# Kernel tuning notes

Measured on AMD Instinct MI355X. Metric: run time of the kernel, lower is better.

The kernel has to match this reference:

```python
import jax, jax.numpy as jnp
import numpy as np
import math

HIDDEN = 128
NUM_HEADS = 8
HEAD_DIM = HIDDEN // NUM_HEADS
B, L = 2, 512


def setup_inputs() -> dict:
    key = jax.random.key(0)
    ks = jax.random.split(key, 14)
    s = 1.0 / math.sqrt(HIDDEN)
    return {
        "x": jax.random.normal(ks[0], (B, L, HIDDEN), jnp.float32),
        "time_k": jax.random.normal(ks[1], (B, L, L, HIDDEN), jnp.float32) * 0.1,
        "time_v": jax.random.normal(ks[2], (B, L, L, HIDDEN), jnp.float32) * 0.1,
        "abs_pos_k": jax.random.normal(ks[3], (B, L, HIDDEN), jnp.float32),
        "abs_pos_v": jax.random.normal(ks[4], (B, L, HIDDEN), jnp.float32),
        "attn_mask": jax.random.normal(ks[5], (B, 1, L, L), jnp.float32),
        "Wq": jax.random.normal(ks[6], (HIDDEN, HIDDEN), jnp.float32) * s,
        "bq": jnp.zeros((HIDDEN,), jnp.float32),
        "Wk": jax.random.normal(ks[7], (HIDDEN, HIDDEN), jnp.float32) * s,
        "bk": jnp.zeros((HIDDEN,), jnp.float32),
        "Wv": jax.random.normal(ks[8], (HIDDEN, HIDDEN), jnp.float32) * s,
        "bv": jnp.zeros((HIDDEN,), jnp.float32),
        "Wo": jax.random.normal(ks[9], (HIDDEN, HIDDEN), jnp.float32) * s,
        "bo": jnp.zeros((HIDDEN,), jnp.float32),
    }


def _split_heads(t):  # [B,L,H] -> [B,nh,L,hd]
    b, l, _ = t.shape
    return t.reshape(b, l, NUM_HEADS, HEAD_DIM).transpose(0, 2, 1, 3)


def reference(x, time_k, time_v, abs_pos_k, abs_pos_v, attn_mask,
              Wq, bq, Wk, bk, Wv, bv, Wo, bo):
    b, l, h = x.shape
    q = _split_heads(x @ Wq + bq)
    k = _split_heads(x @ Wk + bk)
    v = _split_heads(x @ Wv + bv)
    abs_k = _split_heads(abs_pos_k)
    abs_v = _split_heads(abs_pos_v)
    # time biases: [B,L,L,H] -> [B,nh,Lq,Lk,hd]
    tk = time_k.reshape(b, l, l, NUM_HEADS, HEAD_DIM).transpose(0, 3, 1, 2, 4)
    tv = time_v.reshape(b, l, l, NUM_HEADS, HEAD_DIM).transpose(0, 3, 1, 2, 4)
    scores = (
        jnp.einsum("bhqd,bhkd->bhqk", q, k)
        + jnp.einsum("bhqd,bhkd->bhqk", q, abs_k)
        + jnp.einsum("bhqd,bhqkd->bhqk", q, tk)
    ) / math.sqrt(HEAD_DIM)
    scores = scores + attn_mask
    probs = jax.nn.softmax(scores, axis=-1)  # dropout_prob=0 -> identity
    ctx = (
        jnp.einsum("bhqk,bhkd->bhqd", probs, v)
        + jnp.einsum("bhqk,bhkd->bhqd", probs, abs_v)
        + jnp.einsum("bhqk,bhqkd->bhqd", probs, tv)
    )
    ctx = ctx.transpose(0, 2, 1, 3).reshape(b, l, h)
    return ctx @ Wo + bo
```

## Files before the change

kernel.cpp:

```cpp
#include <hip/hip_runtime.h>

#define BB 2
#define LL 512
#define HH 128
#define NH 8
#define SP_STRIDE 9

typedef float f32x4 __attribute__((ext_vector_type(4)));

__global__ __launch_bounds__(128) void qkv_proj_kernel(
    const float* __restrict__ x,
    const float* __restrict__ abs_pos_k,
    const float* __restrict__ abs_pos_v,
    const float* __restrict__ Wq, const float* __restrict__ bq,
    const float* __restrict__ Wk, const float* __restrict__ bk,
    const float* __restrict__ Wv, const float* __restrict__ bv,
    float* __restrict__ q, float* __restrict__ kp, float* __restrict__ vp)
{
    const int r0 = blockIdx.x * 4;
    const int c = threadIdx.x;
    __shared__ float xs[4][HH];
    #pragma unroll
    for (int r = 0; r < 4; ++r) xs[r][c] = x[(r0 + r) * HH + c];
    __syncthreads();
    float aq[4], ak[4], av[4];
    #pragma unroll
    for (int r = 0; r < 4; ++r) { aq[r] = bq[c]; ak[r] = bk[c]; av[r] = bv[c]; }
    #pragma unroll 4
    for (int i = 0; i < HH; ++i) {
        const float wq = Wq[i * HH + c];
        const float wk = Wk[i * HH + c];
        const float wv = Wv[i * HH + c];
        #pragma unroll
        for (int r = 0; r < 4; ++r) {
            const float xv = xs[r][i];
            aq[r] = fmaf(xv, wq, aq[r]);
            ak[r] = fmaf(xv, wk, ak[r]);
            av[r] = fmaf(xv, wv, av[r]);
        }
    }
    #pragma unroll
    for (int r = 0; r < 4; ++r) {
        const int idx = (r0 + r) * HH + c;
        q[idx]  = aq[r];
        kp[idx] = ak[r] + abs_pos_k[idx];
        vp[idx] = av[r] + abs_pos_v[idx];
    }
}

__global__ __launch_bounds__(256) void attn_fused_kernel(
    const float* __restrict__ q,
    const float* __restrict__ kp,
    const float* __restrict__ vp,
    const float* __restrict__ time_k,
    const float* __restrict__ time_v,
    const float* __restrict__ mask,
    const float* __restrict__ Wo,
    const float* __restrict__ bo,
    float* __restrict__ out)
{
    const int blk = blockIdx.x;
    const int b   = blk >> 9;
    const int qi  = blk & (LL - 1);
    const int t   = threadIdx.x;
    const int c4  = t & 31;
    const int kis = t >> 5;
    const int h   = c4 >> 2;

    __shared__ float s_p[LL * SP_STRIDE];
    __shared__ float s_q[HH];
    __shared__ float s_red[8][HH];
    __shared__ float s_ctx[HH];
    __shared__ float s_inv[NH];

    if (t < HH) s_q[t] = q[(b * LL + qi) * HH + t];
    __syncthreads();

    const float4 q4 = ((const float4*)s_q)[c4];
    const f32x4* __restrict__ tk4 = (const f32x4*)(time_k + (size_t)(b * LL + qi) * (size_t)(LL * HH));
    const float4* __restrict__ kq4 = (const float4*)(kp + (size_t)b * (size_t)(LL * HH));
    const float*  __restrict__ mrow = mask + (size_t)(b * LL + qi) * LL;

    #pragma unroll 8
    for (int kb = 0; kb < LL / 8; ++kb) {
        const int ki = kb * 8 + kis;
        const f32x4  a  = __builtin_nontemporal_load(tk4 + ki * 32 + c4);
        const float4 bk = kq4[ki * 32 + c4];
        float part = q4.x * (a.x + bk.x) + q4.y * (a.y + bk.y)
                   + q4.z * (a.z + bk.z) + q4.w * (a.w + bk.w);
        part += __shfl_xor(part, 1);
        part += __shfl_xor(part, 2);
        if ((c4 & 3) == 0)
            s_p[ki * SP_STRIDE + h] = part;
    }
    __syncthreads();

    {
        const int hh  = t >> 5;
        const int l32 = t & 31;
        float v[LL / 32];
        float m = -1e30f;
        #pragma unroll
        for (int j = 0; j < LL / 32; ++j) {
            const int ki = l32 + j * 32;
            v[j] = s_p[ki * SP_STRIDE + hh] * 0.25f + mrow[ki];
            m = fmaxf(m, v[j]);
        }
        #pragma unroll
        for (int off = 16; off; off >>= 1) m = fmaxf(m, __shfl_xor(m, off));
        float sum = 0.f;
        #pragma unroll
        for (int j = 0; j < LL / 32; ++j) {
            const float e = __expf(v[j] - m);
            s_p[(l32 + j * 32) * SP_STRIDE + hh] = e;
            sum += e;
        }
        #pragma unroll
        for (int off = 16; off; off >>= 1) sum += __shfl_xor(sum, off);
        if (l32 == 0) s_inv[hh] = 1.0f / sum;
    }
    __syncthreads();

    const f32x4* __restrict__ tv4 = (const f32x4*)(time_v + (size_t)(b * LL + qi) * (size_t)(LL * HH));
    const float4* __restrict__ vq4 = (const float4*)(vp + (size_t)b * (size_t)(LL * HH));
    float4 acc = make_float4(0.f, 0.f, 0.f, 0.f);
    #pragma unroll 8
    for (int kb = 0; kb < LL / 8; ++kb) {
        const int ki = kb * 8 + kis;
        const float p = s_p[ki * SP_STRIDE + h];
        const f32x4  a  = __builtin_nontemporal_load(tv4 + ki * 32 + c4);
        const float4 bv = vq4[ki * 32 + c4];
        acc.x = fmaf(p, a.x + bv.x, acc.x);
        acc.y = fmaf(p, a.y + bv.y, acc.y);
        acc.z = fmaf(p, a.z + bv.z, acc.z);
        acc.w = fmaf(p, a.w + bv.w, acc.w);
    }
    const float inv = s_inv[h];
    ((float4*)s_red)[kis * 32 + c4] = make_float4(acc.x * inv, acc.y * inv, acc.z * inv, acc.w * inv);
    __syncthreads();

    if (t < HH) {
        float cv = 0.f;
        #pragma unroll
        for (int r = 0; r < 8; ++r) cv += s_red[r][t];
        s_ctx[t] = cv;
    }
    __syncthreads();

    {
        const int to   = t & (HH - 1);
        const int half = t >> 7;
        float o = half ? 0.f : bo[to];
        const int i0 = half * (HH / 2);
        #pragma unroll 4
        for (int i = i0; i < i0 + HH / 2; ++i)
            o = fmaf(s_ctx[i], Wo[i * HH + to], o);
        __syncthreads();
        s_red[half][to] = o;
    }
    __syncthreads();
    if (t < HH)
        out[(b * LL + qi) * HH + t] = s_red[0][t] + s_red[1][t];
}

extern "C" void kernel_launch(void* const* d_in, const int* in_sizes, int n_in,
                              void* d_out, int out_size, void* d_ws, size_t ws_size,
                              hipStream_t stream) {
    const float* x         = (const float*)d_in[0];
    const float* time_k    = (const float*)d_in[1];
    const float* time_v    = (const float*)d_in[2];
    const float* abs_pos_k = (const float*)d_in[3];
    const float* abs_pos_v = (const float*)d_in[4];
    const float* attn_mask = (const float*)d_in[5];
    const float* Wq = (const float*)d_in[6];
    const float* bq = (const float*)d_in[7];
    const float* Wk = (const float*)d_in[8];
    const float* bk = (const float*)d_in[9];
    const float* Wv = (const float*)d_in[10];
    const float* bv = (const float*)d_in[11];
    const float* Wo = (const float*)d_in[12];
    const float* bo = (const float*)d_in[13];
    float* out = (float*)d_out;

    float* q  = (float*)d_ws;
    float* kp = q  + BB * LL * HH;
    float* vp = kp + BB * LL * HH;

    qkv_proj_kernel<<<BB * LL / 4, 128, 0, stream>>>(
        x, abs_pos_k, abs_pos_v, Wq, bq, Wk, bk, Wv, bv, q, kp, vp);

    attn_fused_kernel<<<BB * LL, 256, 0, stream>>>(
        q, kp, vp, time_k, time_v, attn_mask, Wo, bo, out);
}
```

Before: 531.5 us.

## Split fused attention into score, context and output-projection kernels across key halves

Breaks the fused per-query kernel into three kernels. The score and context kernels each split the key dimension into two halves, which doubles the block count, and the raw scores and partial contexts are staged through workspace memory. The aim is more parallelism and memory-level concurrency when streaming the large time_k/time_v tensors. In exchange it adds two kernel launches and global round trips for the scores (8 MB) and partial contexts, and the softmax is recomputed in both halves. The fused kernel is kept as a fallback when the workspace is too small.

```diff
diff --git a/kernel.cpp b/kernel.cpp
--- a/kernel.cpp
+++ b/kernel.cpp
@@ -46,6 +46,176 @@
         kp[idx] = ak[r] + abs_pos_k[idx];
         vp[idx] = av[r] + abs_pos_v[idx];
     }
+}
+
+__global__ __launch_bounds__(256) void score_kernel(
+    const float* __restrict__ q,
+    const float* __restrict__ kp,
+    const float* __restrict__ time_k,
+    float* __restrict__ scores)
+{
+    const int half = blockIdx.x & 1;
+    const int row  = blockIdx.x >> 1;
+    const int b    = row >> 9;
+    const int t    = threadIdx.x;
+    const int c4   = t & 31;
+    const int kis  = t >> 5;
+    const int h    = c4 >> 2;
+
+    __shared__ float s_q[HH];
+    __shared__ float s_p[(LL / 2) * SP_STRIDE];
+
+    if (t < HH) s_q[t] = q[row * HH + t];
+    __syncthreads();
+
+    const float4 q4 = ((const float4*)s_q)[c4];
+    const f32x4*  __restrict__ tk4 = (const f32x4*)(time_k
+        + (size_t)row * (size_t)(LL * HH) + (size_t)half * (LL / 2) * HH);
+    const float4* __restrict__ kq4 = (const float4*)(kp
+        + (size_t)b * (size_t)(LL * HH) + (size_t)half * (LL / 2) * HH);
+
+    #pragma unroll 8
+    for (int kb = 0; kb < LL / 2 / 8; ++kb) {
+        const int ki = kb * 8 + kis;
+        const f32x4  a  = __builtin_nontemporal_load(tk4 + ki * 32 + c4);
+        const float4 bk = kq4[ki * 32 + c4];
+        float part = q4.x * (a.x + bk.x) + q4.y * (a.y + bk.y)
+                   + q4.z * (a.z + bk.z) + q4.w * (a.w + bk.w);
+        part += __shfl_xor(part, 1);
+        part += __shfl_xor(part, 2);
+        if ((c4 & 3) == 0)
+            s_p[ki * SP_STRIDE + h] = part;
+    }
+    __syncthreads();
+
+    float buf[8];
+    #pragma unroll
+    for (int j = 0; j < 8; ++j) {
+        const int idx = t * 8 + j;
+        buf[j] = s_p[(idx >> 3) * SP_STRIDE + (idx & 7)];
+    }
+    float4* dst = (float4*)(scores + (size_t)row * (LL * NH) + half * (LL / 2) * NH + t * 8);
+    dst[0] = make_float4(buf[0], buf[1], buf[2], buf[3]);
+    dst[1] = make_float4(buf[4], buf[5], buf[6], buf[7]);
+}
+
+__global__ __launch_bounds__(256) void ctx_kernel(
+    const float* __restrict__ scores,
+    const float* __restrict__ vp,
+    const float* __restrict__ time_v,
+    const float* __restrict__ mask,
+    float* __restrict__ pctx)
+{
+    const int half = blockIdx.x & 1;
+    const int row  = blockIdx.x >> 1;
+    const int b    = row >> 9;
+    const int t    = threadIdx.x;
+    const int c4   = t & 31;
+    const int kis  = t >> 5;
+    const int h    = c4 >> 2;
+
+    __shared__ float s_p[LL * SP_STRIDE];
+    __shared__ float s_red[8][HH];
+    __shared__ float s_inv[NH];
+
+    {
+        const float4* src = (const float4*)(scores + (size_t)row * (LL * NH));
+        #pragma unroll
+        for (int j = 0; j < 4; ++j) {
+            const float4 v4 = src[t * 4 + j];
+            const int idx = t * 16 + j * 4;
+            s_p[((idx + 0) >> 3) * SP_STRIDE + ((idx + 0) & 7)] = v4.x;
+            s_p[((idx + 1) >> 3) * SP_STRIDE + ((idx + 1) & 7)] = v4.y;
+            s_p[((idx + 2) >> 3) * SP_STRIDE + ((idx + 2) & 7)] = v4.z;
+            s_p[((idx + 3) >> 3) * SP_STRIDE + ((idx + 3) & 7)] = v4.w;
+        }
+    }
+    __syncthreads();
+
+    {
+        const float* __restrict__ mrow = mask + (size_t)row * LL;
+        const int hh  = t >> 5;
+        const int l32 = t & 31;
+        float v[LL / 32];
+        float m = -1e30f;
+        #pragma unroll
+        for (int j = 0; j < LL / 32; ++j) {
+            const int ki = l32 + j * 32;
+            v[j] = s_p[ki * SP_STRIDE + hh] * 0.25f + mrow[ki];
+            m = fmaxf(m, v[j]);
+        }
+        #pragma unroll
+        for (int off = 16; off; off >>= 1) m = fmaxf(m, __shfl_xor(m, off));
+        float sum = 0.f;
+        #pragma unroll
+        for (int j = 0; j < LL / 32; ++j) {
+            const float e = __expf(v[j] - m);
+            s_p[(l32 + j * 32) * SP_STRIDE + hh] = e;
+            sum += e;
+        }
+        #pragma unroll
+        for (int off = 16; off; off >>= 1) sum += __shfl_xor(sum, off);
+        if (l32 == 0) s_inv[hh] = 1.0f / sum;
+    }
+    __syncthreads();
+
+    const f32x4*  __restrict__ tv4 = (const f32x4*)(time_v
+        + (size_t)row * (size_t)(LL * HH) + (size_t)half * (LL / 2) * HH);
+    const float4* __restrict__ vq4 = (const float4*)(vp
+        + (size_t)b * (size_t)(LL * HH) + (size_t)half * (LL / 2) * HH);
+    float4 acc = make_float4(0.f, 0.f, 0.f, 0.f);
+    #pragma unroll 8
+    for (int kb = 0; kb < LL / 2 / 8; ++kb) {
+        const int ki = kb * 8 + kis;
+        const float p = s_p[(half * (LL / 2) + ki) * SP_STRIDE + h];
+        const f32x4  a  = __builtin_nontemporal_load(tv4 + ki * 32 + c4);
+        const float4 bv = vq4[ki * 32 + c4];
+        acc.x = fmaf(p, a.x + bv.x, acc.x);
+        acc.y = fmaf(p, a.y + bv.y, acc.y);
+        acc.z = fmaf(p, a.z + bv.z, acc.z);
+        acc.w = fmaf(p, a.w + bv.w, acc.w);
+    }
+    const float inv = s_inv[h];
+    ((float4*)s_red)[kis * 32 + c4] = make_float4(acc.x * inv, acc.y * inv, acc.z * inv, acc.w * inv);
+    __syncthreads();
+
+    if (t < HH) {
+        float cv = 0.f;
+        #pragma unroll
+        for (int r = 0; r < 8; ++r) cv += s_red[r][t];
+        pctx[(size_t)half * (BB * LL * HH) + (size_t)row * HH + t] = cv;
+    }
+}
+
+__global__ __launch_bounds__(256) void out_proj_kernel(
+    const float* __restrict__ pctx,
+    const float* __restrict__ Wo,
+    const float* __restrict__ bo,
+    float* __restrict__ out)
+{
+    const int row = blockIdx.x;
+    const int t   = threadIdx.x;
+    __shared__ float s_ctx[HH];
+    __shared__ float s_red[2][HH];
+
+    if (t < HH)
+        s_ctx[t] = pctx[(size_t)row * HH + t]
+                 + pctx[(size_t)(BB * LL * HH) + (size_t)row * HH + t];
+    __syncthreads();
+
+    {
+        const int to   = t & (HH - 1);
+        const int half = t >> 7;
+        float o = half ? 0.f : bo[to];
+        const int i0 = half * (HH / 2);
+        #pragma unroll 4
+        for (int i = i0; i < i0 + HH / 2; ++i)
+            o = fmaf(s_ctx[i], Wo[i * HH + to], o);
+        s_red[half][to] = o;
+    }
+    __syncthreads();
+    if (t < HH)
+        out[(size_t)row * HH + t] = s_red[0][t] + s_red[1][t];
 }
 
 __global__ __launch_bounds__(256) void attn_fused_kernel(
@@ -189,6 +359,17 @@
     qkv_proj_kernel<<<BB * LL / 4, 128, 0, stream>>>(
         x, abs_pos_k, abs_pos_v, Wq, bq, Wk, bk, Wv, bv, q, kp, vp);
 
-    attn_fused_kernel<<<BB * LL, 256, 0, stream>>>(
-        q, kp, vp, time_k, time_v, attn_mask, Wo, bo, out);
-}
+    const size_t need = (size_t)(3 * BB * LL * HH
+                               + (size_t)BB * LL * LL * NH
+                               + 2 * BB * LL * HH) * 4;
+    if (ws_size >= need) {
+        float* scores = vp + BB * LL * HH;
+        float* pctx   = scores + (size_t)BB * LL * LL * NH;
+        score_kernel<<<BB * LL * 2, 256, 0, stream>>>(q, kp, time_k, scores);
+        ctx_kernel<<<BB * LL * 2, 256, 0, stream>>>(scores, vp, time_v, attn_mask, pctx);
+        out_proj_kernel<<<BB * LL, 256, 0, stream>>>(pctx, Wo, bo, out);
+    } else {
+        attn_fused_kernel<<<BB * LL, 256, 0, stream>>>(
+            q, kp, vp, time_k, time_v, attn_mask, Wo, bo, out);
+    }
+}
```

Result: slower. 542.9 us (+2.2%).

## Split attention over two key halves with flash-style partial softmax combine

Applied to the files above, without the earlier changes.

Each query row is now processed by two blocks, one per half of the key range, each computing a local max, sum and unnormalized context that go to workspace. A new combine kernel merges the two halves with log-sum-exp rescaling and then applies the output projection. This doubles the number of blocks and halves the shared memory per block, aiming for more memory-level parallelism on the bandwidth-bound time_k/time_v streams. The cost is an extra kernel launch and a small round trip of partial results through global memory.

```diff
diff --git a/kernel.cpp b/kernel.cpp
--- a/kernel.cpp
+++ b/kernel.cpp
@@ -5,6 +5,7 @@
 #define HH 128
 #define NH 8
 #define SP_STRIDE 9
+#define KHALF 256
 
 typedef float f32x4 __attribute__((ext_vector_type(4)));
 
@@ -48,41 +49,39 @@
     }
 }
 
-__global__ __launch_bounds__(256) void attn_fused_kernel(
+__global__ __launch_bounds__(256) void attn_flash_kernel(
     const float* __restrict__ q,
     const float* __restrict__ kp,
     const float* __restrict__ vp,
     const float* __restrict__ time_k,
     const float* __restrict__ time_v,
     const float* __restrict__ mask,
-    const float* __restrict__ Wo,
-    const float* __restrict__ bo,
-    float* __restrict__ out)
+    float* __restrict__ pctx,
+    float2* __restrict__ msbuf)
 {
-    const int blk = blockIdx.x;
-    const int b   = blk >> 9;
-    const int qi  = blk & (LL - 1);
-    const int t   = threadIdx.x;
-    const int c4  = t & 31;
-    const int kis = t >> 5;
-    const int h   = c4 >> 2;
-
-    __shared__ float s_p[LL * SP_STRIDE];
+    const int half = blockIdx.x & 1;
+    const int row  = blockIdx.x >> 1;
+    const int b    = row >> 9;
+    const int t    = threadIdx.x;
+    const int c4   = t & 31;
+    const int kis  = t >> 5;
+    const int h    = c4 >> 2;
+
     __shared__ float s_q[HH];
+    __shared__ float s_p[KHALF * SP_STRIDE];
     __shared__ float s_red[8][HH];
-    __shared__ float s_ctx[HH];
-    __shared__ float s_inv[NH];
-
-    if (t < HH) s_q[t] = q[(b * LL + qi) * HH + t];
+
+    if (t < HH) s_q[t] = q[row * HH + t];
     __syncthreads();
 
     const float4 q4 = ((const float4*)s_q)[c4];
-    const f32x4* __restrict__ tk4 = (const f32x4*)(time_k + (size_t)(b * LL + qi) * (size_t)(LL * HH));
-    const float4* __restrict__ kq4 = (const float4*)(kp + (size_t)b * (size_t)(LL * HH));
-    const float*  __restrict__ mrow = mask + (size_t)(b * LL + qi) * LL;
+    const f32x4*  __restrict__ tk4 = (const f32x4*)(time_k
+        + (size_t)row * (size_t)(LL * HH) + (size_t)half * KHALF * HH);
+    const float4* __restrict__ kq4 = (const float4*)(kp
+        + (size_t)b * (size_t)(LL * HH) + (size_t)half * KHALF * HH);
 
     #pragma unroll 8
-    for (int kb = 0; kb < LL / 8; ++kb) {
+    for (int kb = 0; kb < KHALF / 8; ++kb) {
         const int ki = kb * 8 + kis;
         const f32x4  a  = __builtin_nontemporal_load(tk4 + ki * 32 + c4);
         const float4 bk = kq4[ki * 32 + c4];
@@ -96,12 +95,13 @@
     __syncthreads();
 
     {
+        const float* __restrict__ mrow = mask + (size_t)row * LL + half * KHALF;
         const int hh  = t >> 5;
         const int l32 = t & 31;
-        float v[LL / 32];
+        float v[KHALF / 32];
         float m = -1e30f;
         #pragma unroll
-        for (int j = 0; j < LL / 32; ++j) {
+        for (int j = 0; j < KHALF / 32; ++j) {
             const int ki = l32 + j * 32;
             v[j] = s_p[ki * SP_STRIDE + hh] * 0.25f + mrow[ki];
             m = fmaxf(m, v[j]);
@@ -110,22 +110,25 @@
         for (int off = 16; off; off >>= 1) m = fmaxf(m, __shfl_xor(m, off));
         float sum = 0.f;
         #pragma unroll
-        for (int j = 0; j < LL / 32; ++j) {
+        for (int j = 0; j < KHALF / 32; ++j) {
             const float e = __expf(v[j] - m);
             s_p[(l32 + j * 32) * SP_STRIDE + hh] = e;
             sum += e;
         }
         #pragma unroll
         for (int off = 16; off; off >>= 1) sum += __shfl_xor(sum, off);
-        if (l32 == 0) s_inv[hh] = 1.0f / sum;
-    }
-    __syncthreads();
-
-    const f32x4* __restrict__ tv4 = (const f32x4*)(time_v + (size_t)(b * LL + qi) * (size_t)(LL * HH));
-    const float4* __restrict__ vq4 = (const float4*)(vp + (size_t)b * (size_t)(LL * HH));
+        if (l32 == 0)
+            msbuf[((size_t)half * (BB * LL) + row) * NH + hh] = make_float2(m, sum);
+    }
+    __syncthreads();
+
+    const f32x4*  __restrict__ tv4 = (const f32x4*)(time_v
+        + (size_t)row * (size_t)(LL * HH) + (size_t)half * KHALF * HH);
+    const float4* __restrict__ vq4 = (const float4*)(vp
+        + (size_t)b * (size_t)(LL * HH) + (size_t)half * KHALF * HH);
     float4 acc = make_float4(0.f, 0.f, 0.f, 0.f);
     #pragma unroll 8
-    for (int kb = 0; kb < LL / 8; ++kb) {
+    for (int kb = 0; kb < KHALF / 8; ++kb) {
         const int ki = kb * 8 + kis;
         const float p = s_p[ki * SP_STRIDE + h];
         const f32x4  a  = __builtin_nontemporal_load(tv4 + ki * 32 + c4);
@@ -135,15 +138,40 @@
         acc.z = fmaf(p, a.z + bv.z, acc.z);
         acc.w = fmaf(p, a.w + bv.w, acc.w);
     }
-    const float inv = s_inv[h];
-    ((float4*)s_red)[kis * 32 + c4] = make_float4(acc.x * inv, acc.y * inv, acc.z * inv, acc.w * inv);
+    ((float4*)s_red)[kis * 32 + c4] = acc;
     __syncthreads();
 
     if (t < HH) {
         float cv = 0.f;
         #pragma unroll
         for (int r = 0; r < 8; ++r) cv += s_red[r][t];
-        s_ctx[t] = cv;
+        pctx[(size_t)half * (BB * LL * HH) + (size_t)row * HH + t] = cv;
+    }
+}
+
+__global__ __launch_bounds__(256) void combine_kernel(
+    const float* __restrict__ pctx,
+    const float2* __restrict__ msbuf,
+    const float* __restrict__ Wo,
+    const float* __restrict__ bo,
+    float* __restrict__ out)
+{
+    const int row = blockIdx.x;
+    const int t   = threadIdx.x;
+    __shared__ float s_ctx[HH];
+    __shared__ float s_red[2][HH];
+
+    if (t < HH) {
+        const int h = t >> 4;
+        const float2 ms0 = msbuf[(size_t)row * NH + h];
+        const float2 ms1 = msbuf[(size_t)(BB * LL + row) * NH + h];
+        const float M  = fmaxf(ms0.x, ms1.x);
+        const float e0 = __expf(ms0.x - M);
+        const float e1 = __expf(ms1.x - M);
+        const float denom = ms0.y * e0 + ms1.y * e1;
+        const float p0 = pctx[(size_t)row * HH + t];
+        const float p1 = pctx[(size_t)(BB * LL * HH) + (size_t)row * HH + t];
+        s_ctx[t] = (p0 * e0 + p1 * e1) / denom;
     }
     __syncthreads();
 
@@ -155,12 +183,11 @@
         #pragma unroll 4
         for (int i = i0; i < i0 + HH / 2; ++i)
             o = fmaf(s_ctx[i], Wo[i * HH + to], o);
-        __syncthreads();
         s_red[half][to] = o;
     }
     __syncthreads();
     if (t < HH)
-        out[(b * LL + qi) * HH + t] = s_red[0][t] + s_red[1][t];
+        out[(size_t)row * HH + t] = s_red[0][t] + s_red[1][t];
 }
 
 extern "C" void kernel_launch(void* const* d_in, const int* in_sizes, int n_in,
@@ -182,13 +209,17 @@
     const float* bo = (const float*)d_in[13];
     float* out = (float*)d_out;
 
-    float* q  = (float*)d_ws;
-    float* kp = q  + BB * LL * HH;
-    float* vp = kp + BB * LL * HH;
+    float*  q     = (float*)d_ws;
+    float*  kp    = q  + BB * LL * HH;
+    float*  vp    = kp + BB * LL * HH;
+    float*  pctx  = vp + BB * LL * HH;
+    float2* msbuf = (float2*)(pctx + 2 * BB * LL * HH);
 
     qkv_proj_kernel<<<BB * LL / 4, 128, 0, stream>>>(
         x, abs_pos_k, abs_pos_v, Wq, bq, Wk, bk, Wv, bv, q, kp, vp);
 
-    attn_fused_kernel<<<BB * LL, 256, 0, stream>>>(
-        q, kp, vp, time_k, time_v, attn_mask, Wo, bo, out);
-}
+    attn_flash_kernel<<<BB * LL * 2, 256, 0, stream>>>(
+        q, kp, vp, time_k, time_v, attn_mask, pctx, msbuf);
+
+    combine_kernel<<<BB * LL, 256, 0, stream>>>(pctx, msbuf, Wo, bo, out);
+}
```

Result: no change. 530.7 us (-0.1%).
